# Optimization experiments

Measured on AMD Instinct MI355X. Metric: run time of the kernel, lower is better.

The kernel has to match this reference:

```python
import jax, jax.numpy as jnp
import numpy as np

UNITS = 32
WIDTH = 64
EPS = 1e-7  # keras.backend.epsilon()


def setup_inputs() -> dict:
    key = jax.random.key(0)
    ks = jax.random.split(key, 6)
    B, L, D = 4, 1024, 128
    x = jax.random.normal(ks[0], (B, L, D), dtype=jnp.float32)
    # glorot-normal-ish scaled params
    Wt = jax.random.normal(ks[1], (D, UNITS), dtype=jnp.float32) * (1.0 / np.sqrt(D))
    Wx = jax.random.normal(ks[2], (D, UNITS), dtype=jnp.float32) * (1.0 / np.sqrt(D))
    bh = jnp.zeros((UNITS,), dtype=jnp.float32)
    Wa = jax.random.normal(ks[3], (UNITS, 1), dtype=jnp.float32) * (1.0 / np.sqrt(UNITS))
    ba = jnp.zeros((1,), dtype=jnp.float32)
    return {"x": x, "Wt": Wt, "Wx": Wx, "bh": bh, "Wa": Wa, "ba": ba}


def reference(x, Wt, Wx, bh, Wa, ba):
    # Additive (Bahdanau-style) self-attention emission.
    B, L, D = x.shape
    q = jnp.einsum('bld,du->blu', x, Wt)  # [B,L,U]
    k = jnp.einsum('bld,du->blu', x, Wx)  # [B,L,U]
    # h: [B, Lq, Lk, U] -- dominant intermediate
    h = jnp.tanh(q[:, :, None, :] + k[:, None, :, :] + bh)
    e = jnp.einsum('bqku,u->bqk', h, Wa[:, 0]) + ba[0]  # [B,L,L]
    # stable exp (unnormalized softmax numerator)
    e = jnp.exp(e - jnp.max(e, axis=-1, keepdims=True))
    # local window mask: lower = i - width//2 ; keep lower <= j < lower + width
    idx = jnp.arange(L)
    lower = idx[:, None] - WIDTH // 2
    win = ((lower <= idx[None, :]) & (idx[None, :] < lower + WIDTH)).astype(e.dtype)
    e = e * win
    a = e / (jnp.sum(e, axis=-1, keepdims=True) + EPS)  # [B,L,L]
    v = jnp.einsum('bqk,bkd->bqd', a, x)  # [B,L,D]
    return v
```

## Files before the change

kernel.cpp:

```cpp
#include <hip/hip_runtime.h>
#include <math.h>

#define BB 4
#define LL 1024
#define DD 128
#define UU 32
#define WW 64
#define HALF 32

__global__ __launch_bounds__(256) void qk_kernel(
    const float* __restrict__ x, const float* __restrict__ Wt,
    const float* __restrict__ Wx, const float* __restrict__ bh,
    float* __restrict__ q, float* __restrict__ kT)
{
    __shared__ float xs[4][DD];
    const int tid = threadIdx.x;
    const int w = tid >> 6, lane = tid & 63;
    const int row = blockIdx.x * 4 + w;
    const float* xr = x + (size_t)row * DD;
    xs[w][lane]      = xr[lane];
    xs[w][lane + 64] = xr[lane + 64];
    __syncthreads();
    const int u = lane & 31;
    const bool isQ = (lane < 32);
    const float* Wm = isQ ? Wt : Wx;
    float acc = 0.f;
    #pragma unroll 8
    for (int d = 0; d < DD; ++d)
        acc = fmaf(xs[w][d], Wm[d * UU + u], acc);
    if (isQ) {
        q[(size_t)row * UU + u] = acc + bh[u];
    } else {
        const int b = row >> 10, l = row & (LL - 1);
        kT[((size_t)(b * UU + u)) * LL + l] = acc;
    }
}

__global__ __launch_bounds__(256) void attn_kernel(
    const float* __restrict__ x, const float* __restrict__ q,
    const float* __restrict__ kT, const float* __restrict__ Wa,
    float* __restrict__ out)
{
    __shared__ float qs[4][UU];
    __shared__ float as[4][WW];
    __shared__ float was[UU];
    const int tid = threadIdx.x;
    const int w = tid >> 6, lane = tid & 63;
    if (tid < UU) was[tid] = Wa[tid];
    const int row = blockIdx.x * 4 + w;
    const int b = row >> 10, i = row & (LL - 1);
    if (lane < UU) qs[w][lane] = q[(size_t)row * UU + lane];
    __syncthreads();

    const int j = i - HALF + lane;
    const bool valid = (j >= 0) && (j < LL);
    const int jc = min(max(j, 0), LL - 1);

    float e;
    {
        float acc = 0.f;
        const float* kp = kT + (size_t)b * UU * LL + jc;
        #pragma unroll
        for (int u = 0; u < UU; ++u) {
            float t = qs[w][u] + kp[(size_t)u * LL];
            float ex = __expf(2.f * t);
            float th = fmaf(-2.f, __builtin_amdgcn_rcpf(ex + 1.f), 1.f);
            acc = fmaf(was[u], th, acc);
        }
        e = valid ? acc : -INFINITY;
    }

    float m = e;
    #pragma unroll
    for (int off = 32; off > 0; off >>= 1)
        m = fmaxf(m, __shfl_xor(m, off));
    float p = valid ? __expf(e - m) : 0.f;
    float s = p;
    #pragma unroll
    for (int off = 32; off > 0; off >>= 1)
        s += __shfl_xor(s, off);
    const float a = p / (s + 1e-7f);
    as[w][lane] = a;
    __syncthreads();

    const float* xb = x + (size_t)(b * LL) * DD;
    float v0 = 0.f, v1 = 0.f;
    const int j0 = i - HALF;
    #pragma unroll 8
    for (int l = 0; l < WW; ++l) {
        const float al = as[w][l];
        const int jl = j0 + l;
        const int jlc = min(max(jl, 0), LL - 1);
        const float* xr = xb + (size_t)jlc * DD;
        v0 = fmaf(al, xr[lane], v0);
        v1 = fmaf(al, xr[lane + 64], v1);
    }
    float* o = out + (size_t)row * DD;
    o[lane]      = v0;
    o[lane + 64] = v1;
}

extern "C" void kernel_launch(void* const* d_in, const int* in_sizes, int n_in,
                              void* d_out, int out_size, void* d_ws, size_t ws_size,
                              hipStream_t stream) {
    const float* x  = (const float*)d_in[0];
    const float* Wt = (const float*)d_in[1];
    const float* Wx = (const float*)d_in[2];
    const float* bh = (const float*)d_in[3];
    const float* Wa = (const float*)d_in[4];
    float* out = (float*)d_out;

    float* q  = (float*)d_ws;
    float* kT = q + (size_t)BB * LL * UU;

    const int rows = BB * LL;
    qk_kernel<<<rows / 4, 256, 0, stream>>>(x, Wt, Wx, bh, q, kT);
    attn_kernel<<<rows / 4, 256, 0, stream>>>(x, q, kT, Wa, out);
}
```

Before: 79.88 us.

## Tile attention over 8 query rows with shared-memory staged x and kT windows

```diff
diff --git a/kernel.cpp b/kernel.cpp
--- a/kernel.cpp
+++ b/kernel.cpp
@@ -18,8 +18,7 @@
     const int w = tid >> 6, lane = tid & 63;
     const int row = blockIdx.x * 4 + w;
     const float* xr = x + (size_t)row * DD;
-    xs[w][lane]      = xr[lane];
-    xs[w][lane + 64] = xr[lane + 64];
+    if (lane < 32) ((float4*)xs[w])[lane] = ((const float4*)xr)[lane];
     __syncthreads();
     const int u = lane & 31;
     const bool isQ = (lane < 32);
@@ -36,68 +35,92 @@
     }
 }
 
+#define RPB 8
+#define XR  71
+#define XRP 72
+
 __global__ __launch_bounds__(256) void attn_kernel(
     const float* __restrict__ x, const float* __restrict__ q,
     const float* __restrict__ kT, const float* __restrict__ Wa,
     float* __restrict__ out)
 {
-    __shared__ float qs[4][UU];
-    __shared__ float as[4][WW];
+    __shared__ float xs[XRP][DD];
+    __shared__ float kts[UU][XRP];
+    __shared__ float qs[RPB][UU];
     __shared__ float was[UU];
+    __shared__ float as[4][2][WW];
+
     const int tid = threadIdx.x;
-    const int w = tid >> 6, lane = tid & 63;
+    const int blk = blockIdx.x;
+    const int b  = blk >> 7;
+    const int i0 = (blk & 127) * RPB;
+    const int j0 = i0 - HALF;
+
+    const float* xb = x + (size_t)b * LL * DD;
+
+    {
+        const float4* xb4 = (const float4*)xb;
+        for (int s = tid; s < XRP * (DD / 4); s += 256) {
+            const int r = s >> 5;
+            const int c = s & 31;
+            int jg = j0 + r; jg = min(max(jg, 0), LL - 1);
+            ((float4*)xs)[s] = xb4[jg * (DD / 4) + c];
+        }
+    }
+    {
+        const float* kb = kT + (size_t)b * UU * LL;
+        for (int s = tid; s < UU * XRP; s += 256) {
+            const int u = s / XRP;
+            const int r = s - u * XRP;
+            int jg = j0 + r; jg = min(max(jg, 0), LL - 1);
+            kts[u][r] = kb[(size_t)u * LL + jg];
+        }
+    }
+    ((float*)qs)[tid] = q[((size_t)(b * LL + i0)) * UU + tid];
     if (tid < UU) was[tid] = Wa[tid];
-    const int row = blockIdx.x * 4 + w;
-    const int b = row >> 10, i = row & (LL - 1);
-    if (lane < UU) qs[w][lane] = q[(size_t)row * UU + lane];
     __syncthreads();
 
-    const int j = i - HALF + lane;
-    const bool valid = (j >= 0) && (j < LL);
-    const int jc = min(max(j, 0), LL - 1);
+    const int w = tid >> 6, lane = tid & 63;
 
-    float e;
-    {
+    #pragma unroll
+    for (int rr = 0; rr < 2; ++rr) {
+        const int ir = w * 2 + rr;
+        const int i  = i0 + ir;
+        const int j  = i - HALF + lane;
+        const bool valid = (j >= 0) && (j < LL);
+
         float acc = 0.f;
-        const float* kp = kT + (size_t)b * UU * LL + jc;
         #pragma unroll
         for (int u = 0; u < UU; ++u) {
-            float t = qs[w][u] + kp[(size_t)u * LL];
-            float ex = __expf(2.f * t);
-            float th = fmaf(-2.f, __builtin_amdgcn_rcpf(ex + 1.f), 1.f);
-            acc = fmaf(was[u], th, acc);
+            const float t = qs[ir][u] + kts[u][ir + lane];
+            const float ex = __expf(2.f * t);
+            acc = fmaf(was[u], fmaf(-2.f, __builtin_amdgcn_rcpf(ex + 1.f), 1.f), acc);
         }
-        e = valid ? acc : -INFINITY;
+        const float e = valid ? acc : -INFINITY;
+
+        float m = e;
+        #pragma unroll
+        for (int off = 32; off > 0; off >>= 1)
+            m = fmaxf(m, __shfl_xor(m, off));
+        const float p = valid ? __expf(e - m) : 0.f;
+        float s = p;
+        #pragma unroll
+        for (int off = 32; off > 0; off >>= 1)
+            s += __shfl_xor(s, off);
+        const float a = p * __builtin_amdgcn_rcpf(s + 1e-7f);
+        as[w][rr][lane] = a;
+
+        float v0 = 0.f, v1 = 0.f;
+        #pragma unroll 8
+        for (int l = 0; l < WW; ++l) {
+            const float al = as[w][rr][l];
+            const float2 xv = ((const float2*)xs[ir + l])[lane];
+            v0 = fmaf(al, xv.x, v0);
+            v1 = fmaf(al, xv.y, v1);
+        }
+        float2 o; o.x = v0; o.y = v1;
+        ((float2*)(out + ((size_t)(b * LL + i)) * DD))[lane] = o;
     }
-
-    float m = e;
-    #pragma unroll
-    for (int off = 32; off > 0; off >>= 1)
-        m = fmaxf(m, __shfl_xor(m, off));
-    float p = valid ? __expf(e - m) : 0.f;
-    float s = p;
-    #pragma unroll
-    for (int off = 32; off > 0; off >>= 1)
-        s += __shfl_xor(s, off);
-    const float a = p / (s + 1e-7f);
-    as[w][lane] = a;
-    __syncthreads();
-
-    const float* xb = x + (size_t)(b * LL) * DD;
-    float v0 = 0.f, v1 = 0.f;
-    const int j0 = i - HALF;
-    #pragma unroll 8
-    for (int l = 0; l < WW; ++l) {
-        const float al = as[w][l];
-        const int jl = j0 + l;
-        const int jlc = min(max(jl, 0), LL - 1);
-        const float* xr = xb + (size_t)jlc * DD;
-        v0 = fmaf(al, xr[lane], v0);
-        v1 = fmaf(al, xr[lane + 64], v1);
-    }
-    float* o = out + (size_t)row * DD;
-    o[lane]      = v0;
-    o[lane + 64] = v1;
 }
 
 extern "C" void kernel_launch(void* const* d_in, const int* in_sizes, int n_in,
@@ -113,7 +136,6 @@
     float* q  = (float*)d_ws;
     float* kT = q + (size_t)BB * LL * UU;
 
-    const int rows = BB * LL;
-    qk_kernel<<<rows / 4, 256, 0, stream>>>(x, Wt, Wx, bh, q, kT);
-    attn_kernel<<<rows / 4, 256, 0, stream>>>(x, q, kT, Wa, out);
+    qk_kernel<<<BB * LL / 4, 256, 0, stream>>>(x, Wt, Wx, bh, q, kT);
+    attn_kernel<<<BB * (LL / RPB), 256, 0, stream>>>(x, q, kT, Wa, out);
 }
```

Result: slower. 83.16 us (+4.1%).
